# Performance work log

Hardware: AMD Instinct MI355X
Metric: run time of the kernel (lower is better)

## Reference

```python
import jax, jax.numpy as jnp
import numpy as np


def setup_inputs() -> dict:
    key = jax.random.key(0)
    pred = jax.random.normal(key, (16, 4, 768, 768), dtype=jnp.float32)
    return {"pred": pred}


def _largest_cc(mask):
    """Largest 4-connected component of a 2D boolean mask, as float32 0/1.

    Equivalent to scipy.ndimage.label (default 4-connectivity) followed by
    keeping the largest label. Uses min-label flood propagation: each
    foreground pixel starts with its raster index; iterated neighbor-min
    converges so every pixel holds its component's minimum pixel index
    (the 'root'). Ties in size resolve to the smallest root, which matches
    scipy's label-order tie-breaking (labels assigned in raster order).
    """
    H, W = mask.shape
    HW = H * W
    idx = jnp.arange(HW, dtype=jnp.int32).reshape(H, W)
    BIG = jnp.int32(HW)  # sentinel for background
    lbl0 = jnp.where(mask, idx, BIG)

    def body(carry):
        lbl, _ = carry
        p = jnp.pad(lbl, 1, constant_values=HW)
        nb = jnp.minimum(jnp.minimum(p[:-2, 1:-1], p[2:, 1:-1]),
                         jnp.minimum(p[1:-1, :-2], p[1:-1, 2:]))
        new = jnp.where(mask, jnp.minimum(lbl, nb), BIG)
        return new, jnp.any(new != lbl)

    lbl, _ = jax.lax.while_loop(lambda c: c[1], body, (lbl0, jnp.any(mask)))

    # component sizes keyed by root pixel index; background bucket = HW
    sizes = jax.ops.segment_sum(mask.ravel().astype(jnp.int32), lbl.ravel(),
                                num_segments=HW + 1)
    sizes = sizes.at[HW].set(0)
    root = jnp.argmax(sizes).astype(jnp.int32)
    return ((lbl == root) & mask).astype(jnp.float32)


def reference(pred):
    B, C, H, W = pred.shape
    labels = jnp.argmax(pred, axis=1)  # [B, H, W]
    cls = jnp.arange(1, C, dtype=labels.dtype)
    masks = labels[:, None, :, :] == cls[None, :, None, None]  # [B, C-1, H, W]
    comp = jax.vmap(_largest_cc)(masks.reshape(-1, H, W)).reshape(B, C - 1, H, W)
    bg = 1.0 - jnp.clip(comp.sum(axis=1), 0.0, 1.0)  # channel 0
    return jnp.concatenate([bg[:, None], comp], axis=1)
```

## Files before the change

### kernel.cpp

```cpp
#include <hip/hip_runtime.h>
#include <stdint.h>

#define BB 16
#define CC 4
#define HH 768
#define WW 768
#define HW (HH * WW)
#define NPIX (BB * HW)
#define NIMG (BB * (CC - 1))
#define BEST_STRIDE 16

#define TS 64
#define TPI (WW / TS)
#define TILES_PER_IMG (TPI * TPI)
#define TPIX (TS * TS)
#define CCL_TPB 256
#define STRIP 16

typedef unsigned long long ull;


__device__ __forceinline__ int find_root(int* P, int i) {
    int p = P[i];
    while (p != i) {
        int gp = P[p];
        P[i] = gp;
        i = p;
        p = gp;
    }
    return i;
}

__device__ __forceinline__ void merge(int* P, int a, int b) {
    a = find_root(P, a);
    b = find_root(P, b);
    while (a != b) {
        if (a < b) { int t = a; a = b; b = t; }
        int old = atomicCAS(&P[a], a, b);
        if (old == a) return;
        a = find_root(P, old);
        b = find_root(P, b);
    }
}


__device__ __forceinline__ int lfind(int* P, int i) {
    int p = P[i];
    while (p != i) {
        int gp = P[p];
        P[i] = gp;
        i = p;
        p = gp;
    }
    return i;
}

__device__ __forceinline__ void lmerge(int* P, int a, int b) {
    a = lfind(P, a);
    b = lfind(P, b);
    while (a != b) {
        if (a < b) { int t = a; a = b; b = t; }
        int old = atomicCAS(&P[a], a, b);
        if (old == a) return;
        a = lfind(P, old);
        b = lfind(P, b);
    }
}

__device__ __forceinline__ ull umax64(ull a, ull b) { return a > b ? a : b; }

__device__ __forceinline__ void lds_fence() {
    asm volatile("s_waitcnt lgkmcnt(0)" ::: "memory");
    __builtin_amdgcn_sched_barrier(0);
}


__global__ __launch_bounds__(CCL_TPB) void k_tile_ccl(
        const float* __restrict__ pred,
        uint8_t* __restrict__ labels,
        int* __restrict__ parent,
        uint32_t* __restrict__ counts,
        ull* __restrict__ best) {
    __shared__ __align__(16) int sp[TPIX];
    __shared__ __align__(16) uint8_t slab[TPIX];

    if (blockIdx.x == 0) {
        for (int i = threadIdx.x; i < NIMG * BEST_STRIDE; i += CCL_TPB) best[i] = 0ull;
    }

    const int tid = (int)threadIdx.x;
    const int img = blockIdx.x / TILES_PER_IMG;
    const int tile = blockIdx.x % TILES_PER_IMG;
    const int tr = (tile / TPI) * TS;
    const int tc = (tile % TPI) * TS;
    const float* pb = pred + (size_t)img * CC * HW;
    const int imgbase = img * HW;

    for (int k = 0; k < TPIX; k += CCL_TPB * 4) {
        int li = k + tid * 4;
        int gi = (tr + (li >> 6)) * WW + tc + (li & 63);
        float4 v0 = *(const float4*)&pb[gi];
        float4 v1 = *(const float4*)&pb[gi + HW];
        float4 v2 = *(const float4*)&pb[gi + 2 * HW];
        float4 v3 = *(const float4*)&pb[gi + 3 * HW];
        const float* a0 = &v0.x; const float* a1 = &v1.x;
        const float* a2 = &v2.x; const float* a3 = &v3.x;
        uchar4 lout;
        uint8_t* lj = &lout.x;
        #pragma unroll
        for (int j = 0; j < 4; ++j) {
            int lab = 0;
            float bv = a0[j];
            if (a1[j] > bv) { bv = a1[j]; lab = 1; }
            if (a2[j] > bv) { bv = a2[j]; lab = 2; }
            if (a3[j] > bv) { bv = a3[j]; lab = 3; }
            lj[j] = (uint8_t)lab;
        }
        *(uchar4*)&slab[li] = lout;
        *(uchar4*)&labels[imgbase + gi] = lout;
    }
    __syncthreads();

    const int w = tid >> 6;
    const int lane = tid & 63;

    {
        int prevLab = 0, prevV = 0;
        #pragma unroll 1
        for (int r = 0; r < STRIP; ++r) {
            int row = (w << 4) + r;
            int li = (row << 6) + lane;
            int lab = slab[li];
            int labL = __shfl_up(lab, 1, 64);
            bool isStart = lab && (lane == 0 || labL != lab);
            ull mask = __ballot(isStart);
            int v = li;
            if (lab) {
                ull mle = mask & (~0ull >> (63 - lane));
                v = (row << 6) + (63 - __clzll(mle));
            }
            sp[li] = v;
            lds_fence();
            if (r > 0) {
                int labUL = __shfl_up(prevLab, 1, 64);
                if (lab && prevLab == lab) {
                    if (lane == 0 || !(labL == lab && labUL == lab))
                        lmerge(sp, v, prevV);
                }
            }
            prevLab = lab;
            prevV = v;
        }
    }
    __syncthreads();

    if (tid < 64 * 3) {
        int row = ((tid >> 6) + 1) << 4;
        int c = tid & 63;
        int li = (row << 6) + c;
        int lab = slab[li];
        int labU = slab[li - TS];
        if (lab && labU == lab) {
            bool seg = true;
            if (c > 0) {
                int labL = slab[li - 1];
                int labUL = slab[li - TS - 1];
                seg = !(labL == lab && labUL == lab);
            }
            if (seg) lmerge(sp, li, li - TS);
        }
    }
    __syncthreads();

    #pragma unroll 1
    for (int it = 0; it < TPIX / CCL_TPB; ++it) {
        int li = it * CCL_TPB + tid;
        int c = tid & 63;
        int lab = slab[li];
        int labL = __shfl_up(lab, 1, 64);
        bool isStart = lab && (c == 0 || labL != lab);
        bool isEnd = lab && (c == 63 || (int)slab[li + 1] != lab);
        ull endmask = __ballot(isEnd);
        if (lab) {
            int p = sp[li] & 0xFFFF;
            if (p != li) {
                int q0 = sp[p] & 0xFFFF;
                while (q0 != p) { p = q0; q0 = sp[p] & 0xFFFF; }
                sp[li] = p;
            }
            if (isStart) {
                ull mge = endmask & (~0ull << c);
                int epos = __ffsll((long long)mge) - 1;
                int runlen = epos - c + 1;
                atomicAdd((unsigned int*)&sp[p], (unsigned int)runlen << 16);
            }
        }
    }
    __syncthreads();

    for (int k = 0; k < TPIX; k += CCL_TPB * 4) {
        int li = k + tid * 4;
        int gi = imgbase + (tr + (li >> 6)) * WW + tc + (li & 63);
        uchar4 lv = *(const uchar4*)&slab[li];
        int4 sv = *(const int4*)&sp[li];
        const uint8_t* lj = &lv.x;
        const int* sj = &sv.x;
        int4 pout; uint4 cout;
        int* pj = &pout.x; uint32_t* cj = &cout.x;
        #pragma unroll
        for (int j = 0; j < 4; ++j) {
            int root = sj[j] & 0xFFFF;
            if (lj[j]) {
                pj[j] = imgbase + (tr + (root >> 6)) * WW + tc + (root & 63);
                cj[j] = (root == li + j) ? ((uint32_t)sj[j] >> 16) : 0u;
            } else {
                pj[j] = -1;
                cj[j] = 0u;
            }
        }
        *(int4*)&parent[gi] = pout;
        *(uint4*)&counts[gi] = cout;
    }
}

#define VEDGES ((TPI - 1) * HH)
#define EDGES_PER_IMG (2 * (TPI - 1) * HH)
__global__ void k_border_merge(const uint8_t* __restrict__ labels, int* parent) {
    int t = blockIdx.x * blockDim.x + threadIdx.x;
    if (t >= BB * EDGES_PER_IMG) return;
    int img = t / EDGES_PER_IMG;
    int e = t % EDGES_PER_IMG;
    int a, b;
    if (e < VEDGES) {
        int j = e / HH, r = e % HH;
        int c = j * TS + TS - 1;
        a = r * WW + c;
        b = a + 1;
    } else {
        e -= VEDGES;
        int j = e / WW, c = e % WW;
        int r = j * TS + TS - 1;
        a = r * WW + c;
        b = a + WW;
    }
    int ga = img * HW + a, gb = img * HW + b;
    uint8_t la = labels[ga];
    if (la && labels[gb] == la) merge(parent, ga, gb);
}

__global__ void k_compress(int* __restrict__ parent, uint32_t* __restrict__ counts) {
    int q = blockIdx.x * blockDim.x + threadIdx.x;
    if (q >= NPIX / 4) return;
    int t = q * 4;
    uint4 cv = *(const uint4*)&counts[t];
    if (!(cv.x | cv.y | cv.z | cv.w)) return;
    uint32_t cs[4] = {cv.x, cv.y, cv.z, cv.w};
    #pragma unroll
    for (int j = 0; j < 4; ++j) {
        if (!cs[j]) continue;
        int i = t + j;
        int g = parent[i];
        if (g == i) continue;
        while (true) { int pg = parent[g]; if (pg == g) break; g = pg; }
        parent[i] = g;
        atomicAdd(&counts[g], cs[j]);
        counts[i] = 0;
    }
}

#define BEST_BLK_PER_IMG 144
#define BEST_TPB 256
#define BEST_PIX_PER_BLK (HW / BEST_BLK_PER_IMG)
__global__ void k_best(const uint8_t* __restrict__ labels,
                       const uint32_t* __restrict__ counts,
                       ull* __restrict__ best) {
    __shared__ ull sw[(BEST_TPB / 64) * 3];
    int img = blockIdx.x / BEST_BLK_PER_IMG;
    int chunk = blockIdx.x % BEST_BLK_PER_IMG;
    int base = img * HW + chunk * BEST_PIX_PER_BLK;

    ull l0 = 0, l1 = 0, l2 = 0;
    for (int k = 0; k < BEST_PIX_PER_BLK; k += BEST_TPB * 4) {
        int t = base + k + (int)threadIdx.x * 4;
        uint4 cv = *(const uint4*)&counts[t];
        if (cv.x | cv.y | cv.z | cv.w) {
            uchar4 lv = *(const uchar4*)&labels[t];
            uint32_t cs[4] = {cv.x, cv.y, cv.z, cv.w};
            uint8_t ls[4] = {lv.x, lv.y, lv.z, lv.w};
            #pragma unroll
            for (int j = 0; j < 4; ++j) {
                if (cs[j]) {
                    int cc = (int)ls[j] - 1;
                    ull key = ((ull)cs[j] << 32) | (ull)(~(uint32_t)(t + j));
                    if (cc == 0) l0 = umax64(l0, key);
                    else if (cc == 1) l1 = umax64(l1, key);
                    else l2 = umax64(l2, key);
                }
            }
        }
    }
    #pragma unroll
    for (int m = 1; m < 64; m <<= 1) {
        l0 = umax64(l0, __shfl_xor(l0, m, 64));
        l1 = umax64(l1, __shfl_xor(l1, m, 64));
        l2 = umax64(l2, __shfl_xor(l2, m, 64));
    }
    int lane = threadIdx.x & 63;
    int wid = threadIdx.x >> 6;
    if (lane == 0) { sw[wid * 3 + 0] = l0; sw[wid * 3 + 1] = l1; sw[wid * 3 + 2] = l2; }
    __syncthreads();
    if (threadIdx.x < 3) {
        ull m = 0;
        for (int w = 0; w < BEST_TPB / 64; ++w) m = umax64(m, sw[w * 3 + threadIdx.x]);
        if (m) atomicMax(&best[(img * 3 + (int)threadIdx.x) * BEST_STRIDE], m);
    }
}

__global__ void k_output(const uint8_t* __restrict__ labels,
                         const int* __restrict__ parent,
                         const ull* __restrict__ best,
                         float* __restrict__ out) {
    int q = blockIdx.x * blockDim.x + threadIdx.x;
    if (q >= NPIX / 4) return;
    int t = q * 4;
    int b = t / HW;
    int i = t - b * HW;
    uchar4 lv = *(const uchar4*)&labels[t];
    int4 pv = *(const int4*)&parent[t];
    int root[3];
    root[0] = (int)(~(uint32_t)best[(b * 3 + 0) * BEST_STRIDE]);
    root[1] = (int)(~(uint32_t)best[(b * 3 + 1) * BEST_STRIDE]);
    root[2] = (int)(~(uint32_t)best[(b * 3 + 2) * BEST_STRIDE]);

    uint8_t ls[4] = {lv.x, lv.y, lv.z, lv.w};
    int ps[4] = {pv.x, pv.y, pv.z, pv.w};
    float fg[4];
    #pragma unroll
    for (int j = 0; j < 4; ++j) {
        int g = -1;
        if (ps[j] >= 0) g = parent[ps[j]];
        fg[j] = (ls[j] && g == root[ls[j] - 1]) ? 1.0f : 0.0f;
    }

    float4 o0, o1, o2, o3;
    float* c0 = &o0.x; float* c1 = &o1.x; float* c2 = &o2.x; float* c3 = &o3.x;
    #pragma unroll
    for (int j = 0; j < 4; ++j) {
        c0[j] = 1.0f - fg[j];
        c1[j] = (ls[j] == 1) ? fg[j] : 0.0f;
        c2[j] = (ls[j] == 2) ? fg[j] : 0.0f;
        c3[j] = (ls[j] == 3) ? fg[j] : 0.0f;
    }
    float* o = out + (size_t)b * CC * HW + i;
    *(float4*)&o[0] = o0;
    *(float4*)&o[HW] = o1;
    *(float4*)&o[2 * HW] = o2;
    *(float4*)&o[3 * HW] = o3;
}


extern "C" void kernel_launch(void* const* d_in, const int* in_sizes, int n_in,
                              void* d_out, int out_size, void* d_ws, size_t ws_size,
                              hipStream_t stream) {
    const float* pred = (const float*)d_in[0];
    float* out = (float*)d_out;

    uint8_t* labels = (uint8_t*)d_ws;
    int* parent = (int*)((char*)d_ws + NPIX);
    ull* best = (ull*)((char*)d_ws + NPIX + (size_t)NPIX * 4);
    uint32_t* counts = (uint32_t*)d_out;

    const int TPB = 256;

    k_tile_ccl<<<BB * TILES_PER_IMG, CCL_TPB, 0, stream>>>(pred, labels, parent, counts, best);
    k_border_merge<<<(BB * EDGES_PER_IMG + TPB - 1) / TPB, TPB, 0, stream>>>(labels, parent);
    k_compress<<<(NPIX / 4 + TPB - 1) / TPB, TPB, 0, stream>>>(parent, counts);
    k_best<<<BB * BEST_BLK_PER_IMG, BEST_TPB, 0, stream>>>(labels, counts, best);
    k_output<<<(NPIX / 4 + TPB - 1) / TPB, TPB, 0, stream>>>(labels, parent, best, out);
}
```

Measured before the change: 150.1 us.

## Switch tile CCL to independent per-wave 16x64 strips without block barriers

Local labeling now gives each wavefront its own 16x64 strip in LDS, replacing the 64x64 tile shared by four waves. This removes the block-wide __syncthreads calls and the in-tile stitching pass between strips, leaving only wave-local LDS fences. The cost is more strip borders: horizontal edges every 16 rows are now merged in the global border-merge kernel with global atomics. That adds global union-find work and can deepen the trees that compress has to walk.

```diff
diff --git a/kernel.cpp b/kernel.cpp
--- a/kernel.cpp
+++ b/kernel.cpp
@@ -10,12 +10,14 @@
 #define NIMG (BB * (CC - 1))
 #define BEST_STRIDE 16
 
-#define TS 64
-#define TPI (WW / TS)
-#define TILES_PER_IMG (TPI * TPI)
-#define TPIX (TS * TS)
-#define CCL_TPB 256
-#define STRIP 16
+#define SH 16
+#define SW 64
+#define SPIX (SH * SW)
+#define SX (WW / SW)
+#define SY (HH / SH)
+#define SPI (SX * SY)
+#define WPB 4
+#define CCL_TPB (WPB * 64)
 
 typedef unsigned long long ull;
 
@@ -75,29 +77,35 @@
 }
 
 
-__global__ __launch_bounds__(CCL_TPB) void k_tile_ccl(
+__global__ __launch_bounds__(CCL_TPB) void k_strip_ccl(
         const float* __restrict__ pred,
         uint8_t* __restrict__ labels,
         int* __restrict__ parent,
         uint32_t* __restrict__ counts,
         ull* __restrict__ best) {
-    __shared__ __align__(16) int sp[TPIX];
-    __shared__ __align__(16) uint8_t slab[TPIX];
+    __shared__ __align__(16) int sp_all[WPB][SPIX];
+    __shared__ __align__(16) uint8_t slab_all[WPB][SPIX];
 
     if (blockIdx.x == 0) {
         for (int i = threadIdx.x; i < NIMG * BEST_STRIDE; i += CCL_TPB) best[i] = 0ull;
     }
 
     const int tid = (int)threadIdx.x;
-    const int img = blockIdx.x / TILES_PER_IMG;
-    const int tile = blockIdx.x % TILES_PER_IMG;
-    const int tr = (tile / TPI) * TS;
-    const int tc = (tile % TPI) * TS;
+    const int w = tid >> 6;
+    const int lane = tid & 63;
+    int* sp = sp_all[w];
+    uint8_t* slab = slab_all[w];
+
+    const int gs = blockIdx.x * WPB + w;
+    const int img = gs / SPI;
+    const int s = gs % SPI;
+    const int tr = (s / SX) * SH;
+    const int tc = (s % SX) * SW;
     const float* pb = pred + (size_t)img * CC * HW;
     const int imgbase = img * HW;
 
-    for (int k = 0; k < TPIX; k += CCL_TPB * 4) {
-        int li = k + tid * 4;
+    for (int it = 0; it < 4; ++it) {
+        int li = it * 256 + lane * 4;
         int gi = (tr + (li >> 6)) * WW + tc + (li & 63);
         float4 v0 = *(const float4*)&pb[gi];
         float4 v1 = *(const float4*)&pb[gi + HW];
@@ -119,17 +127,13 @@
         *(uchar4*)&slab[li] = lout;
         *(uchar4*)&labels[imgbase + gi] = lout;
     }
-    __syncthreads();
-
-    const int w = tid >> 6;
-    const int lane = tid & 63;
+    lds_fence();
 
     {
         int prevLab = 0, prevV = 0;
         #pragma unroll 1
-        for (int r = 0; r < STRIP; ++r) {
-            int row = (w << 4) + r;
-            int li = (row << 6) + lane;
+        for (int r = 0; r < SH; ++r) {
+            int li = (r << 6) + lane;
             int lab = slab[li];
             int labL = __shfl_up(lab, 1, 64);
             bool isStart = lab && (lane == 0 || labL != lab);
@@ -137,49 +141,28 @@
             int v = li;
             if (lab) {
                 ull mle = mask & (~0ull >> (63 - lane));
-                v = (row << 6) + (63 - __clzll(mle));
+                v = (r << 6) + (63 - __clzll(mle));
             }
             sp[li] = v;
             lds_fence();
-            if (r > 0) {
-                int labUL = __shfl_up(prevLab, 1, 64);
-                if (lab && prevLab == lab) {
-                    if (lane == 0 || !(labL == lab && labUL == lab))
-                        lmerge(sp, v, prevV);
-                }
+            int labUL = __shfl_up(prevLab, 1, 64);
+            if (r > 0 && lab && prevLab == lab) {
+                if (lane == 0 || !(labL == lab && labUL == lab))
+                    lmerge(sp, v, prevV);
             }
             prevLab = lab;
             prevV = v;
         }
     }
-    __syncthreads();
-
-    if (tid < 64 * 3) {
-        int row = ((tid >> 6) + 1) << 4;
-        int c = tid & 63;
-        int li = (row << 6) + c;
-        int lab = slab[li];
-        int labU = slab[li - TS];
-        if (lab && labU == lab) {
-            bool seg = true;
-            if (c > 0) {
-                int labL = slab[li - 1];
-                int labUL = slab[li - TS - 1];
-                seg = !(labL == lab && labUL == lab);
-            }
-            if (seg) lmerge(sp, li, li - TS);
-        }
-    }
-    __syncthreads();
+    lds_fence();
 
     #pragma unroll 1
-    for (int it = 0; it < TPIX / CCL_TPB; ++it) {
-        int li = it * CCL_TPB + tid;
-        int c = tid & 63;
+    for (int r = 0; r < SH; ++r) {
+        int li = (r << 6) + lane;
         int lab = slab[li];
         int labL = __shfl_up(lab, 1, 64);
-        bool isStart = lab && (c == 0 || labL != lab);
-        bool isEnd = lab && (c == 63 || (int)slab[li + 1] != lab);
+        bool isStart = lab && (lane == 0 || labL != lab);
+        bool isEnd = lab && (lane == 63 || (int)slab[li + 1] != lab);
         ull endmask = __ballot(isEnd);
         if (lab) {
             int p = sp[li] & 0xFFFF;
@@ -189,17 +172,17 @@
                 sp[li] = p;
             }
             if (isStart) {
-                ull mge = endmask & (~0ull << c);
+                ull mge = endmask & (~0ull << lane);
                 int epos = __ffsll((long long)mge) - 1;
-                int runlen = epos - c + 1;
+                int runlen = epos - lane + 1;
                 atomicAdd((unsigned int*)&sp[p], (unsigned int)runlen << 16);
             }
         }
     }
-    __syncthreads();
-
-    for (int k = 0; k < TPIX; k += CCL_TPB * 4) {
-        int li = k + tid * 4;
+    lds_fence();
+
+    for (int it = 0; it < 4; ++it) {
+        int li = it * 256 + lane * 4;
         int gi = imgbase + (tr + (li >> 6)) * WW + tc + (li & 63);
         uchar4 lv = *(const uchar4*)&slab[li];
         int4 sv = *(const int4*)&sp[li];
@@ -223,23 +206,24 @@
     }
 }
 
-#define VEDGES ((TPI - 1) * HH)
-#define EDGES_PER_IMG (2 * (TPI - 1) * HH)
+#define VED ((SX - 1) * HH)
+#define HED ((SY - 1) * WW)
+#define EPI (VED + HED)
 __global__ void k_border_merge(const uint8_t* __restrict__ labels, int* parent) {
     int t = blockIdx.x * blockDim.x + threadIdx.x;
-    if (t >= BB * EDGES_PER_IMG) return;
-    int img = t / EDGES_PER_IMG;
-    int e = t % EDGES_PER_IMG;
+    if (t >= BB * EPI) return;
+    int img = t / EPI;
+    int e = t % EPI;
     int a, b;
-    if (e < VEDGES) {
+    if (e < VED) {
         int j = e / HH, r = e % HH;
-        int c = j * TS + TS - 1;
+        int c = (j + 1) * SW - 1;
         a = r * WW + c;
         b = a + 1;
     } else {
-        e -= VEDGES;
+        e -= VED;
         int j = e / WW, c = e % WW;
-        int r = j * TS + TS - 1;
+        int r = (j + 1) * SH - 1;
         a = r * WW + c;
         b = a + WW;
     }
@@ -372,8 +356,8 @@
 
     const int TPB = 256;
 
-    k_tile_ccl<<<BB * TILES_PER_IMG, CCL_TPB, 0, stream>>>(pred, labels, parent, counts, best);
-    k_border_merge<<<(BB * EDGES_PER_IMG + TPB - 1) / TPB, TPB, 0, stream>>>(labels, parent);
+    k_strip_ccl<<<BB * SPI / WPB, CCL_TPB, 0, stream>>>(pred, labels, parent, counts, best);
+    k_border_merge<<<(BB * EPI + TPB - 1) / TPB, TPB, 0, stream>>>(labels, parent);
     k_compress<<<(NPIX / 4 + TPB - 1) / TPB, TPB, 0, stream>>>(parent, counts);
     k_best<<<BB * BEST_BLK_PER_IMG, BEST_TPB, 0, stream>>>(labels, counts, best);
     k_output<<<(NPIX / 4 + TPB - 1) / TPB, TPB, 0, stream>>>(labels, parent, best, out);
```

After: 155.9 us. 3.8% more time.
